# Optimization experiments

Measured on AMD Instinct MI355X. Metric: run time of the kernel, lower is better.

## Reference

```python
import jax, jax.numpy as jnp
import numpy as np

B, S, D, H = 2, 4096, 1024, 16
DK = D // H


def setup_inputs() -> dict:
    key = jax.random.key(0)
    ks = jax.random.split(key, 8)
    q = jax.random.normal(ks[0], (B, S, D), dtype=jnp.float32)
    k = jax.random.normal(ks[1], (B, S, D), dtype=jnp.float32)
    v = jax.random.normal(ks[2], (B, S, D), dtype=jnp.float32)
    mask = jax.random.randint(ks[3], (1, 1, S, S), 0, 2, dtype=jnp.int32)
    # torch.nn.Linear weights, y = x @ W.T ; Kaiming-uniform-ish init scale
    lim = 1.0 / np.sqrt(D)
    Wq = jax.random.uniform(ks[4], (D, D), jnp.float32, -lim, lim)
    Wk = jax.random.uniform(ks[5], (D, D), jnp.float32, -lim, lim)
    Wv = jax.random.uniform(ks[6], (D, D), jnp.float32, -lim, lim)
    Wo = jax.random.uniform(ks[7], (D, D), jnp.float32, -lim, lim)
    return {"q": q, "k": k, "v": v, "mask": mask,
            "Wq": Wq, "Wk": Wk, "Wv": Wv, "Wo": Wo}


def reference(q, k, v, mask, Wq, Wk, Wv, Wo):
    # Linear projections (torch Linear: x @ W.T), split into heads [B,H,S,DK]
    def heads(x, W):
        return (x @ W.T).reshape(B, S, H, DK).transpose(0, 2, 1, 3)

    Q, K, V = heads(q, Wq), heads(k, Wk), heads(v, Wv)
    scale = 1.0 / jnp.sqrt(jnp.asarray(DK, dtype=Q.dtype))
    # [B,H,S,S] score matrix (original materializes it fully)
    scores = jnp.einsum("bhqd,bhkd->bhqk", Q, K) * scale
    # NOTE: original calls masked_fill without assignment -> mask is a no-op.
    # Dropout: eval-mode identity (original also references missing self.dropout).
    attn = jax.nn.softmax(scores, axis=-1)
    out = jnp.einsum("bhqk,bhkd->bhqd", attn, V)  # [B,H,S,DK]
    out = out.transpose(0, 2, 1, 3).reshape(B, S, D)
    return out @ Wo.T
```

## Files before the change

kernel.cpp:

```cpp
#include <hip/hip_runtime.h>
#include <cstdint>
#include <cstddef>

using u16 = unsigned short;
using u32 = unsigned int;

typedef _Float16 f16x8 __attribute__((ext_vector_type(8)));
typedef float    f32x4 __attribute__((ext_vector_type(4)));
typedef float    f32x16 __attribute__((ext_vector_type(16)));

#define MFMA16(a,b,c) __builtin_amdgcn_mfma_f32_16x16x32_f16((a),(b),(c),0,0,0)
#define MFMA32(a,b,c) __builtin_amdgcn_mfma_f32_32x32x16_f16((a),(b),(c),0,0,0)
#define SGB __builtin_amdgcn_sched_group_barrier

__device__ __forceinline__ u16 f2h(float f) {
  return __builtin_bit_cast(u16, (_Float16)f);
}
__device__ __forceinline__ u32 pkrtz(float a, float b) {
  return __builtin_bit_cast(u32, __builtin_amdgcn_cvt_pkrtz(a, b));
}
__device__ __forceinline__ void plswap(u32 &a, u32 &b) {
  asm volatile("v_permlane32_swap_b32 %0, %1" : "+v"(a), "+v"(b));
}
__device__ __forceinline__ void async16(const void* g, void* lds) {
  __builtin_amdgcn_global_load_lds((const __attribute__((address_space(1))) void*)g,
                                   (__attribute__((address_space(3))) void*)lds,
                                   16, 0, 0);
}
#if __has_builtin(__builtin_amdgcn_exp2f)
__device__ __forceinline__ float exp2_hw(float x) { return __builtin_amdgcn_exp2f(x); }
#else
__device__ __forceinline__ float exp2_hw(float x) {
  float r; asm("v_exp_f32 %0, %1" : "=v"(r) : "v"(x)); return r;
}
#endif

__global__ __launch_bounds__(256) void cvt4_w(const float* __restrict__ w0,
                                              const float* __restrict__ w1,
                                              const float* __restrict__ w2,
                                              const float* __restrict__ w3,
                                              u16* __restrict__ d0, u16* __restrict__ d1,
                                              u16* __restrict__ d2, u16* __restrict__ d3,
                                              int n4, float scale0) {
  const int y = blockIdx.y;
  const float* in = y == 0 ? w0 : (y == 1 ? w1 : (y == 2 ? w2 : w3));
  u16* out = y == 0 ? d0 : (y == 1 ? d1 : (y == 2 ? d2 : d3));
  const float sc = y == 0 ? scale0 : 1.0f;
  int i = blockIdx.x * 256 + threadIdx.x;
  const int stride = gridDim.x * 256;
  for (; i < n4; i += stride) {
    const float4 f = reinterpret_cast<const float4*>(in)[i];
    ushort4 o;
    o.x = f2h(f.x * sc); o.y = f2h(f.y * sc);
    o.z = f2h(f.z * sc); o.w = f2h(f.w * sc);
    reinterpret_cast<ushort4*>(out)[i] = o;
  }
}

__global__ __launch_bounds__(256) void cvt3_x(const float* __restrict__ q,
                                              const float* __restrict__ k,
                                              const float* __restrict__ v,
                                              u16* __restrict__ xq, u16* __restrict__ xk,
                                              u16* __restrict__ xv, int n4) {
  const int y = blockIdx.y;
  const float* in = y == 0 ? q : (y == 1 ? k : v);
  u16* out = y == 0 ? xq : (y == 1 ? xk : xv);
  int i = blockIdx.x * 256 + threadIdx.x;
  const int stride = gridDim.x * 256;
  for (; i < n4; i += stride) {
    const float4 f = reinterpret_cast<const float4*>(in)[i];
    ushort4 o;
    o.x = f2h(f.x); o.y = f2h(f.y); o.z = f2h(f.z); o.w = f2h(f.w);
    reinterpret_cast<ushort4*>(out)[i] = o;
  }
}

template <int OF32>
__device__ __forceinline__ void gemm_body(const u16* __restrict__ A,
                                          const u16* __restrict__ Bw,
                                          float* __restrict__ Cf,
                                          u16* __restrict__ Ch,
                                          int m0, int n0, int N, int K) {
  __shared__ __align__(16) u16 Asm[128 * 64];
  __shared__ __align__(16) u16 Bsm[128 * 64];
  const int tid = threadIdx.x;
  const int w = tid >> 6, l = tid & 63;
  const int wr = w >> 1, wc = w & 1;
  const int lr = l >> 3, lc = l & 7, csrc = lc ^ lr;
  const int laneq = l & 15, laneg = l >> 4;
  f32x4 acc[4][4] = {};
  for (int k0 = 0; k0 < K; k0 += 64) {
    __syncthreads();
#pragma unroll
    for (int c = 0; c < 4; ++c) {
      const int row = c * 32 + w * 8 + lr;
      async16(A + (size_t)(m0 + row) * K + k0 + csrc * 8, &Asm[c * 2048 + w * 512]);
      async16(Bw + (size_t)(n0 + row) * K + k0 + csrc * 8, &Bsm[c * 2048 + w * 512]);
    }
    __syncthreads();
#pragma unroll
    for (int ks = 0; ks < 2; ++ks) {
      f16x8 af[4], bfr[4];
#pragma unroll
      for (int mi = 0; mi < 4; ++mi) {
        const int row = wr * 64 + mi * 16 + laneq;
        const int ch = (ks * 4 + laneg) ^ (row & 7);
        af[mi] = *(const f16x8*)&Asm[row * 64 + ch * 8];
      }
#pragma unroll
      for (int ni = 0; ni < 4; ++ni) {
        const int row = wc * 64 + ni * 16 + laneq;
        const int ch = (ks * 4 + laneg) ^ (row & 7);
        bfr[ni] = *(const f16x8*)&Bsm[row * 64 + ch * 8];
      }
#pragma unroll
      for (int mi = 0; mi < 4; ++mi)
#pragma unroll
        for (int ni = 0; ni < 4; ++ni)
          acc[mi][ni] = MFMA16(af[mi], bfr[ni], acc[mi][ni]);
    }
  }
#pragma unroll
  for (int mi = 0; mi < 4; ++mi)
#pragma unroll
    for (int r = 0; r < 4; ++r) {
      const int gm = m0 + wr * 64 + mi * 16 + laneg * 4 + r;
#pragma unroll
      for (int ni = 0; ni < 4; ++ni) {
        const int gn = n0 + wc * 64 + ni * 16 + laneq;
        if constexpr (OF32) Cf[(size_t)gm * N + gn] = acc[mi][ni][r];
        else                Ch[(size_t)gm * N + gn] = f2h(acc[mi][ni][r]);
      }
    }
}

__global__ __launch_bounds__(256) void gemm_qk(const u16* __restrict__ xq,
                                               const u16* __restrict__ wq,
                                               u16* __restrict__ Qp,
                                               const u16* __restrict__ xk,
                                               const u16* __restrict__ wk,
                                               u16* __restrict__ Kp) {
  const bool zk = blockIdx.z != 0;
  gemm_body<0>(zk ? xk : xq, zk ? wk : wq, nullptr, zk ? Kp : Qp,
               blockIdx.y * 128, blockIdx.x * 128, 1024, 1024);
}

__global__ __launch_bounds__(256) void gemm_vt(const u16* __restrict__ wv,
                                               const u16* __restrict__ xv,
                                               u16* __restrict__ VT) {
  gemm_body<0>(wv, xv, nullptr, VT, blockIdx.y * 128, blockIdx.x * 128, 8192, 1024);
}

__global__ __launch_bounds__(256) void gemm_f(const u16* __restrict__ A,
                                              const u16* __restrict__ Bw,
                                              float* __restrict__ Cf,
                                              int N, int K) {
  gemm_body<1>(A, Bw, Cf, nullptr, blockIdx.y * 128, blockIdx.x * 128, N, K);
}

__global__ __launch_bounds__(256, 4) void attn_fwd(const u16* __restrict__ Qp,
                                                   const u16* __restrict__ Kp,
                                                   const u16* __restrict__ VT,
                                                   u16* __restrict__ AO) {
  union SM {
    struct { u16 K[2][64 * 64]; u16 V[2][64 * 64]; } st;
    u16 osm[4][32 * 72];
  };
  __shared__ __align__(16) SM sm;
  const int tid = threadIdx.x, w = tid >> 6, l = tid & 63;
  const int l31 = l & 31, hi = l >> 5, l7 = l & 7, lr = l >> 3;
  const int bid = blockIdx.x;
  const int slot = bid >> 3;
  const int bh = (bid & 7) * 4 + (slot >> 5), qx = slot & 31;
  const int b = bh >> 4, h = bh & 15;
  const int q0 = qx * 128;
  const size_t hb = (size_t)b * 4096 * 1024 + (size_t)h * 64;
  const u16* Kh = Kp + hb;
  const u16* Vh = VT + (size_t)h * 64 * 8192 + (size_t)b * 4096;
  const int csrc = l7 ^ lr;

  f16x8 qf[4];
  {
    const u16* qp = Qp + hb + (size_t)(q0 + w * 32 + l31) * 1024 + hi * 8;
#pragma unroll
    for (int kk = 0; kk < 4; ++kk) qf[kk] = *(const f16x8*)(qp + kk * 16);
  }

  f32x16 zero16;
#pragma unroll
  for (int r = 0; r < 16; ++r) zero16[r] = 0.f;

  f32x16 acc[2];
#pragma unroll
  for (int r = 0; r < 16; ++r) { acc[0][r] = 0.f; acc[1][r] = 0.f; }
  float lp0 = 0.f, lp1 = 0.f, lp2 = 0.f, lp3 = 0.f;

  int koff = (w * 8 + lr) * 1024 + csrc * 8;
  int voff = (w * 8 + lr) * 8192 + csrc * 8;

  async16(Kh + koff,             &sm.st.K[0][w * 512]);
  async16(Kh + koff + 32 * 1024, &sm.st.K[0][w * 512 + 2048]);
  async16(Vh + voff,             &sm.st.V[0][w * 512]);
  async16(Vh + voff + 32 * 8192, &sm.st.V[0][w * 512 + 2048]);

  for (int t = 0; t < 64; ++t) {
    const int cur = t & 1;
    __syncthreads();
    const u16* Ks = sm.st.K[cur];
    const u16* Vs = sm.st.V[cur];

    __builtin_amdgcn_s_setprio(1);
    f32x16 sv;
    {
      f16x8 kf = *(const f16x8*)&Ks[l31 * 64 + ((hi ^ l7) << 3)];
      sv = MFMA32(kf, qf[0], zero16);
#pragma unroll
      for (int kk = 1; kk < 4; ++kk) {
        kf = *(const f16x8*)&Ks[l31 * 64 + (((kk * 2 + hi) ^ l7) << 3)];
        sv = MFMA32(kf, qf[kk], sv);
      }
    }
    __builtin_amdgcn_s_setprio(0);
    if (t < 63) {
      koff += 64 * 1024;
      voff += 64;
      async16(Kh + koff,             &sm.st.K[cur ^ 1][w * 512]);
      async16(Kh + koff + 32 * 1024, &sm.st.K[cur ^ 1][w * 512 + 2048]);
      async16(Vh + voff,             &sm.st.V[cur ^ 1][w * 512]);
      async16(Vh + voff + 32 * 8192, &sm.st.V[cur ^ 1][w * 512 + 2048]);
    }

    f16x8 pf0[2];
#pragma unroll
    for (int r = 0; r < 16; ++r) sv[r] = exp2_hw(sv[r]);
    lp0 += sv[0] + sv[4];  lp1 += sv[1] + sv[5];
    lp2 += sv[2] + sv[6];  lp3 += sv[3] + sv[7];
    lp0 += sv[8] + sv[12]; lp1 += sv[9] + sv[13];
    lp2 += sv[10] + sv[14]; lp3 += sv[11] + sv[15];
#pragma unroll
    for (int half = 0; half < 2; ++half) {
      const int rb = half * 8;
      u32 a0 = pkrtz(sv[rb + 0], sv[rb + 1]);
      u32 a1 = pkrtz(sv[rb + 2], sv[rb + 3]);
      u32 b0 = pkrtz(sv[rb + 4], sv[rb + 5]);
      u32 b1 = pkrtz(sv[rb + 6], sv[rb + 7]);
      plswap(a0, b0);
      plswap(a1, b1);
      union { u32 ww[4]; f16x8 v; } uu;
      uu.ww[0] = a0; uu.ww[1] = a1; uu.ww[2] = b0; uu.ww[3] = b1;
      pf0[half] = uu.v;
    }

    {
      f16x8 kf = *(const f16x8*)&Ks[(32 + l31) * 64 + ((hi ^ l7) << 3)];
      sv = MFMA32(kf, qf[0], zero16);
#pragma unroll
      for (int kk = 1; kk < 4; ++kk) {
        kf = *(const f16x8*)&Ks[(32 + l31) * 64 + (((kk * 2 + hi) ^ l7) << 3)];
        sv = MFMA32(kf, qf[kk], sv);
      }
    }

#pragma unroll
    for (int half = 0; half < 2; ++half)
#pragma unroll
      for (int ds = 0; ds < 2; ++ds) {
        const f16x8 vf = *(const f16x8*)&Vs[(ds * 32 + l31) * 64 + (((half * 2 + hi) ^ l7) << 3)];
        acc[ds] = MFMA32(vf, pf0[half], acc[ds]);
      }

    f16x8 pf1[2];
#pragma unroll
    for (int r = 0; r < 16; ++r) sv[r] = exp2_hw(sv[r]);
    lp0 += sv[0] + sv[4];  lp1 += sv[1] + sv[5];
    lp2 += sv[2] + sv[6];  lp3 += sv[3] + sv[7];
    lp0 += sv[8] + sv[12]; lp1 += sv[9] + sv[13];
    lp2 += sv[10] + sv[14]; lp3 += sv[11] + sv[15];
#pragma unroll
    for (int half = 0; half < 2; ++half) {
      const int rb = half * 8;
      u32 a0 = pkrtz(sv[rb + 0], sv[rb + 1]);
      u32 a1 = pkrtz(sv[rb + 2], sv[rb + 3]);
      u32 b0 = pkrtz(sv[rb + 4], sv[rb + 5]);
      u32 b1 = pkrtz(sv[rb + 6], sv[rb + 7]);
      plswap(a0, b0);
      plswap(a1, b1);
      union { u32 ww[4]; f16x8 v; } uu;
      uu.ww[0] = a0; uu.ww[1] = a1; uu.ww[2] = b0; uu.ww[3] = b1;
      pf1[half] = uu.v;
    }

#pragma unroll
    for (int half = 0; half < 2; ++half)
#pragma unroll
      for (int ds = 0; ds < 2; ++ds) {
        const f16x8 vf = *(const f16x8*)&Vs[(ds * 32 + l31) * 64 + (((4 + half * 2 + hi) ^ l7) << 3)];
        acc[ds] = MFMA32(vf, pf1[half], acc[ds]);
      }

    SGB(0x2, 72, 0);
    SGB(0x8, 4, 0);
    SGB(0x100, 2, 0); SGB(0x8, 1, 0); SGB(0x2, 18, 0);
    SGB(0x100, 2, 0); SGB(0x8, 1, 0); SGB(0x2, 18, 0);
    SGB(0x8, 1, 0);   SGB(0x2, 18, 0);
    SGB(0x8, 1, 0);   SGB(0x2, 18, 0);
    SGB(0x100, 4, 0);
    SGB(0x8, 4, 0);
  }
  float ls = (lp0 + lp1) + (lp2 + lp3);
  ls += __shfl_xor(ls, 32);
  __syncthreads();
  {
    const float rn = 1.f / ls;
#pragma unroll
    for (int ds = 0; ds < 2; ++ds)
#pragma unroll
      for (int g = 0; g < 4; ++g) {
        uint2 val;
        val.x = pkrtz(acc[ds][4 * g + 0] * rn, acc[ds][4 * g + 1] * rn);
        val.y = pkrtz(acc[ds][4 * g + 2] * rn, acc[ds][4 * g + 3] * rn);
        *(uint2*)&sm.osm[w][l31 * 72 + ds * 32 + g * 8 + hi * 4] = val;
      }
  }
  asm volatile("s_waitcnt lgkmcnt(0)" ::: "memory");
#pragma unroll
  for (int i = 0; i < 4; ++i) {
    const int row = lr + i * 8;
    const uint4 vv = *(const uint4*)&sm.osm[w][row * 72 + l7 * 8];
    *(uint4*)(AO + hb + (size_t)(q0 + w * 32 + row) * 1024 + l7 * 8) = vv;
  }
}

extern "C" void kernel_launch(void* const* d_in, const int* in_sizes, int n_in,
                              void* d_out, int out_size, void* d_ws, size_t ws_size,
                              hipStream_t stream) {
  const float* q  = (const float*)d_in[0];
  const float* k  = (const float*)d_in[1];
  const float* v  = (const float*)d_in[2];
  const float* Wq = (const float*)d_in[4];
  const float* Wk = (const float*)d_in[5];
  const float* Wv = (const float*)d_in[6];
  const float* Wo = (const float*)d_in[7];
  float* out = (float*)d_out;

  char* ws = (char*)d_ws;
  u16* xq  = (u16*)ws;
  u16* xk  = (u16*)(ws + 16777216);
  u16* xv  = (u16*)(ws + 2 * 16777216);
  u16* Qp  = (u16*)(ws + 3 * 16777216);
  u16* Kpp = (u16*)(ws + 4 * 16777216);
  u16* wqb = (u16*)(ws + 5 * 16777216);
  u16* wkb = wqb + 1048576;
  u16* wvb = wkb + 1048576;
  u16* wob = wvb + 1048576;
  u16* VT  = xq;
  u16* AO  = xv;

  constexpr float SC = 0.125f * 1.44269504088896340736f;
  cvt4_w<<<dim3(256, 4), 256, 0, stream>>>(Wq, Wk, Wv, Wo, wqb, wkb, wvb, wob,
                                           262144, SC);
  cvt3_x<<<dim3(1024, 3), 256, 0, stream>>>(q, k, v, xq, xk, xv, 2097152);

  gemm_qk<<<dim3(8, 64, 2), 256, 0, stream>>>(xq, wqb, Qp, xk, wkb, Kpp);
  gemm_vt<<<dim3(64, 8), 256, 0, stream>>>(wvb, xv, VT);

  attn_fwd<<<1024, 256, 0, stream>>>(Qp, Kpp, VT, AO);

  gemm_f<<<dim3(8, 64), 256, 0, stream>>>(AO, wob, out, 1024, 1024);
}
```

Baseline: 276.5 us.

## Fuse fp32-to-fp16 activation conversion into QKV projection GEMM loads

Removes the separate cvt3_x kernel and makes the projection GEMMs read fp32 activations directly, converting to fp16 in registers before storing to LDS. The Q, K and V projections are merged into a single launch using blockIdx.z. This drops a full write and re-read of the fp16 activation copies and one launch. In exchange the activation tiles are loaded synchronously (plain global loads plus LDS stores) instead of through async copies, at twice the bytes per element, and each tile is re-read once per output block column.

Result: slower. 302.4 us (+9.4%).

```diff
diff --git a/kernel.cpp b/kernel.cpp
--- a/kernel.cpp
+++ b/kernel.cpp
@@ -57,27 +57,9 @@
   }
 }
 
-__global__ __launch_bounds__(256) void cvt3_x(const float* __restrict__ q,
-                                              const float* __restrict__ k,
-                                              const float* __restrict__ v,
-                                              u16* __restrict__ xq, u16* __restrict__ xk,
-                                              u16* __restrict__ xv, int n4) {
-  const int y = blockIdx.y;
-  const float* in = y == 0 ? q : (y == 1 ? k : v);
-  u16* out = y == 0 ? xq : (y == 1 ? xk : xv);
-  int i = blockIdx.x * 256 + threadIdx.x;
-  const int stride = gridDim.x * 256;
-  for (; i < n4; i += stride) {
-    const float4 f = reinterpret_cast<const float4*>(in)[i];
-    ushort4 o;
-    o.x = f2h(f.x); o.y = f2h(f.y); o.z = f2h(f.z); o.w = f2h(f.w);
-    reinterpret_cast<ushort4*>(out)[i] = o;
-  }
-}
-
-template <int OF32>
-__device__ __forceinline__ void gemm_body(const u16* __restrict__ A,
-                                          const u16* __restrict__ Bw,
+template <int OF32, int AF32, int BF32>
+__device__ __forceinline__ void gemm_body(const void* __restrict__ Ap,
+                                          const void* __restrict__ Bp,
                                           float* __restrict__ Cf,
                                           u16* __restrict__ Ch,
                                           int m0, int n0, int N, int K) {
@@ -94,8 +76,31 @@
 #pragma unroll
     for (int c = 0; c < 4; ++c) {
       const int row = c * 32 + w * 8 + lr;
-      async16(A + (size_t)(m0 + row) * K + k0 + csrc * 8, &Asm[c * 2048 + w * 512]);
-      async16(Bw + (size_t)(n0 + row) * K + k0 + csrc * 8, &Bsm[c * 2048 + w * 512]);
+      const int ldsoff = c * 2048 + w * 512 + l * 8;
+      if constexpr (AF32) {
+        const float* src = (const float*)Ap + (size_t)(m0 + row) * K + k0 + csrc * 8;
+        const float4 f0 = *(const float4*)src;
+        const float4 f1 = *(const float4*)(src + 4);
+        union { u16 s[8]; uint4 u; } o;
+        o.s[0] = f2h(f0.x); o.s[1] = f2h(f0.y); o.s[2] = f2h(f0.z); o.s[3] = f2h(f0.w);
+        o.s[4] = f2h(f1.x); o.s[5] = f2h(f1.y); o.s[6] = f2h(f1.z); o.s[7] = f2h(f1.w);
+        *(uint4*)&Asm[ldsoff] = o.u;
+      } else {
+        async16((const u16*)Ap + (size_t)(m0 + row) * K + k0 + csrc * 8,
+                &Asm[c * 2048 + w * 512]);
+      }
+      if constexpr (BF32) {
+        const float* src = (const float*)Bp + (size_t)(n0 + row) * K + k0 + csrc * 8;
+        const float4 f0 = *(const float4*)src;
+        const float4 f1 = *(const float4*)(src + 4);
+        union { u16 s[8]; uint4 u; } o;
+        o.s[0] = f2h(f0.x); o.s[1] = f2h(f0.y); o.s[2] = f2h(f0.z); o.s[3] = f2h(f0.w);
+        o.s[4] = f2h(f1.x); o.s[5] = f2h(f1.y); o.s[6] = f2h(f1.z); o.s[7] = f2h(f1.w);
+        *(uint4*)&Bsm[ldsoff] = o.u;
+      } else {
+        async16((const u16*)Bp + (size_t)(n0 + row) * K + k0 + csrc * 8,
+                &Bsm[c * 2048 + w * 512]);
+      }
     }
     __syncthreads();
 #pragma unroll
@@ -134,28 +139,33 @@
     }
 }
 
-__global__ __launch_bounds__(256) void gemm_qk(const u16* __restrict__ xq,
-                                               const u16* __restrict__ wq,
-                                               u16* __restrict__ Qp,
-                                               const u16* __restrict__ xk,
-                                               const u16* __restrict__ wk,
-                                               u16* __restrict__ Kp) {
-  const bool zk = blockIdx.z != 0;
-  gemm_body<0>(zk ? xk : xq, zk ? wk : wq, nullptr, zk ? Kp : Qp,
-               blockIdx.y * 128, blockIdx.x * 128, 1024, 1024);
-}
-
-__global__ __launch_bounds__(256) void gemm_vt(const u16* __restrict__ wv,
-                                               const u16* __restrict__ xv,
-                                               u16* __restrict__ VT) {
-  gemm_body<0>(wv, xv, nullptr, VT, blockIdx.y * 128, blockIdx.x * 128, 8192, 1024);
+__global__ __launch_bounds__(256) void gemm_qkv(const float* __restrict__ xq,
+                                                const u16* __restrict__ wq,
+                                                u16* __restrict__ Qp,
+                                                const float* __restrict__ xk,
+                                                const u16* __restrict__ wk,
+                                                u16* __restrict__ Kp,
+                                                const float* __restrict__ xv,
+                                                const u16* __restrict__ wv,
+                                                u16* __restrict__ VT) {
+  const int z = blockIdx.z;
+  if (z == 2) {
+    gemm_body<0, 0, 1>(wv, xv, nullptr, VT,
+                       blockIdx.x * 128, blockIdx.y * 128, 8192, 1024);
+  } else if (z == 1) {
+    gemm_body<0, 1, 0>(xk, wk, nullptr, Kp,
+                       blockIdx.y * 128, blockIdx.x * 128, 1024, 1024);
+  } else {
+    gemm_body<0, 1, 0>(xq, wq, nullptr, Qp,
+                       blockIdx.y * 128, blockIdx.x * 128, 1024, 1024);
+  }
 }
 
 __global__ __launch_bounds__(256) void gemm_f(const u16* __restrict__ A,
                                               const u16* __restrict__ Bw,
                                               float* __restrict__ Cf,
                                               int N, int K) {
-  gemm_body<1>(A, Bw, Cf, nullptr, blockIdx.y * 128, blockIdx.x * 128, N, K);
+  gemm_body<1, 0, 0>(A, Bw, Cf, nullptr, blockIdx.y * 128, blockIdx.x * 128, N, K);
 }
 
 __global__ __launch_bounds__(256, 4) void attn_fwd(const u16* __restrict__ Qp,
@@ -344,25 +354,21 @@
   float* out = (float*)d_out;
 
   char* ws = (char*)d_ws;
-  u16* xq  = (u16*)ws;
-  u16* xk  = (u16*)(ws + 16777216);
-  u16* xv  = (u16*)(ws + 2 * 16777216);
-  u16* Qp  = (u16*)(ws + 3 * 16777216);
-  u16* Kpp = (u16*)(ws + 4 * 16777216);
-  u16* wqb = (u16*)(ws + 5 * 16777216);
+  u16* Qp  = (u16*)ws;
+  u16* Kpp = (u16*)(ws + 16777216);
+  u16* VT  = (u16*)(ws + 2 * 16777216);
+  u16* AO  = (u16*)(ws + 3 * 16777216);
+  u16* wqb = (u16*)(ws + 4 * 16777216);
   u16* wkb = wqb + 1048576;
   u16* wvb = wkb + 1048576;
   u16* wob = wvb + 1048576;
-  u16* VT  = xq;
-  u16* AO  = xv;
 
   constexpr float SC = 0.125f * 1.44269504088896340736f;
   cvt4_w<<<dim3(256, 4), 256, 0, stream>>>(Wq, Wk, Wv, Wo, wqb, wkb, wvb, wob,
                                            262144, SC);
-  cvt3_x<<<dim3(1024, 3), 256, 0, stream>>>(q, k, v, xq, xk, xv, 2097152);
-
-  gemm_qk<<<dim3(8, 64, 2), 256, 0, stream>>>(xq, wqb, Qp, xk, wkb, Kpp);
-  gemm_vt<<<dim3(64, 8), 256, 0, stream>>>(wvb, xv, VT);
+
+  gemm_qkv<<<dim3(8, 64, 3), 256, 0, stream>>>(q, wqb, Qp, k, wkb, Kpp,
+                                               v, wvb, VT);
 
   attn_fwd<<<1024, 256, 0, stream>>>(Qp, Kpp, VT, AO);
 
```
